# Optimization experiments

Hardware: AMD Instinct MI355X
Metric: run time of the kernel (lower is better)

Reference implementation:

```python
import jax, jax.numpy as jnp
import numpy as np

MAG = 1.0
TAU = 0.5
B, D, C = 8192, 256, 128


def setup_inputs() -> dict:
    key = jax.random.key(0)
    k1, k2 = jax.random.split(key)
    outputs = jax.random.normal(k1, (B, D), dtype=jnp.float32)
    labels = jax.random.normal(k2, (B, C), dtype=jnp.float32)
    return {"outputs": outputs, "labels": labels}


def reference(outputs, labels):
    # Cosine-similarity matrix of labels, min-max normalized to [0, 1]
    norm2labels = labels / (jnp.linalg.norm(labels, axis=1, keepdims=True) + 1e-12)
    sim_mat = norm2labels @ norm2labels.T  # [B, B]
    sim_mat = (sim_mat - sim_mat.min()) / (sim_mat.max() - sim_mat.min())

    # Pairwise Euclidean distances of outputs via the Gram trick
    # ||x_i - x_j||^2 = ||x_i||^2 + ||x_j||^2 - 2 <x_i, x_j>
    sq = jnp.sum(outputs * outputs, axis=1)  # [B]
    d2 = sq[:, None] + sq[None, :] - 2.0 * (outputs @ outputs.T)  # [B, B]
    d2 = jnp.maximum(d2, 0.0)
    nz = d2 > 0.0
    # safe sqrt: zero (diagonal) entries get distance 0 with zero gradient,
    # matching torch.norm's subgradient at 0
    eud = jnp.sqrt(jnp.where(nz, d2, 1.0)) * nz
    eud = eud / eud.max()

    distance = eud + sim_mat  # [B, B]
    pos_mask = sim_mat > TAU

    # Per-row masked log-sum-exp terms (distance in [0, 2], no overflow risk)
    pos_loss = jnp.log(jnp.sum(jnp.where(pos_mask, jnp.exp(distance), 0.0), axis=1))
    neg_loss = jnp.log(jnp.sum(jnp.where(pos_mask, 0.0, jnp.exp(MAG - distance)), axis=1))

    # clamp negatives (and -inf from empty masks) to 0, as the original `if < 0` does
    loss = jnp.maximum(pos_loss, 0.0) + jnp.maximum(neg_loss, 0.0)
    return jnp.mean(loss)
```

## Files before the change

kernel.cpp:

```cpp
#include <hip/hip_runtime.h>
#include <hip/hip_bf16.h>


#define B_N 8192
#define NT   64
#define TILE 128
#define NTRI 2080

typedef __attribute__((ext_vector_type(8))) short bf16x8;
typedef __attribute__((ext_vector_type(4))) float f32x4;
typedef __attribute__((ext_vector_type(2))) _Float16 f16x2;

typedef const __attribute__((address_space(1))) void g_void;
typedef __attribute__((address_space(3))) void l_void;

__device__ __forceinline__ unsigned fenc(float f) {
    unsigned u = __float_as_uint(f);
    return (u & 0x80000000u) ? ~u : (u | 0x80000000u);
}
__device__ __forceinline__ float fdec(unsigned k) {
    unsigned u = (k & 0x80000000u) ? (k ^ 0x80000000u) : ~k;
    return __uint_as_float(u);
}
__device__ __forceinline__ unsigned pack2(float a, float b) {
    f16x2 p; p[0] = (_Float16)a; p[1] = (_Float16)b;
    return *(unsigned*)&p;
}

__device__ __forceinline__ void tile_decode(int b, int& bi, int& bj) {
    int si, sj, ti, tj;
    if (b < 544) {
        int sb = b / 136, w = b - sb * 136;
        int i = 0;
        while (w >= 16 - i) { w -= 16 - i; i++; }
        si = sb; sj = sb; ti = i; tj = i + w;
    } else {
        int q = (b - 544) >> 8, w = (b - 544) & 255;
        int i = 0;
        while (q >= 3 - i) { q -= 3 - i; i++; }
        si = i; sj = i + 1 + q;
        ti = w >> 4; tj = w & 15;
    }
    bi = si * 16 + ti; bj = sj * 16 + tj;
}

__global__ __launch_bounds__(256) void prep_kernel(
    const float* __restrict__ outputs, const float* __restrict__ labels,
    __hip_bfloat16* __restrict__ Obp, __hip_bfloat16* __restrict__ Lnp,
    float* __restrict__ sq, float* __restrict__ pos_sums,
    float* __restrict__ neg_sums, unsigned* __restrict__ stats) {
    int g = blockIdx.x, tid = threadIdx.x;
    int rl = tid >> 4, c = tid & 15;
    int row = g * 16 + rl;
    __shared__ __align__(16) short tO[16][264];
    __shared__ __align__(16) short tL[16][136];

    float s = 0.f;
    #pragma unroll
    for (int k = 0; k < 4; k++) {
        f32x4 v = *(const f32x4*)&outputs[(size_t)row * 256 + c * 16 + k * 4];
        s += v[0]*v[0] + v[1]*v[1] + v[2]*v[2] + v[3]*v[3];
        __hip_bfloat16 b4[4];
        #pragma unroll
        for (int i = 0; i < 4; i++) b4[i] = __float2bfloat16(v[i]);
        *(uint2*)&tO[rl][c * 16 + k * 4] = *(uint2*)b4;
    }
    #pragma unroll
    for (int m = 1; m < 16; m <<= 1) s += __shfl_xor(s, m);
    if (c == 0) sq[row] = s;

    float ls = 0.f;
    f32x4 u0 = *(const f32x4*)&labels[(size_t)row * 128 + c * 8];
    f32x4 u1 = *(const f32x4*)&labels[(size_t)row * 128 + c * 8 + 4];
    ls += u0[0]*u0[0] + u0[1]*u0[1] + u0[2]*u0[2] + u0[3]*u0[3];
    ls += u1[0]*u1[0] + u1[1]*u1[1] + u1[2]*u1[2] + u1[3]*u1[3];
    #pragma unroll
    for (int m = 1; m < 16; m <<= 1) ls += __shfl_xor(ls, m);
    float inv = 1.f / (sqrtf(ls) + 1e-12f);
    {
        __hip_bfloat16 b4[4];
        #pragma unroll
        for (int i = 0; i < 4; i++) b4[i] = __float2bfloat16(u0[i] * inv);
        *(uint2*)&tL[rl][c * 8] = *(uint2*)b4;
        #pragma unroll
        for (int i = 0; i < 4; i++) b4[i] = __float2bfloat16(u1[i] * inv);
        *(uint2*)&tL[rl][c * 8 + 4] = *(uint2*)b4;
    }
    if (tid < 16) { pos_sums[g * 16 + tid] = 0.f; neg_sums[g * 16 + tid] = 0.f; }
    if (g == 0 && tid == 0) {
        stats[0] = 0xFFFFFFFFu; stats[1] = 0u; stats[2] = 0u;
    }
    __syncthreads();

    #pragma unroll
    for (int q = 0; q < 2; q++) {
        int sl = tid * 2 + q;
        int o = sl >> 4, rr = sl & 15;
        uint4 d = *(uint4*)&tO[rr][o * 8];
        *(uint4*)&Obp[(size_t)g * 4096 + (size_t)sl * 8] = d;
    }
    {
        int o = tid >> 4, rr = tid & 15;
        uint4 d = *(uint4*)&tL[rr][o * 8];
        *(uint4*)&Lnp[(size_t)g * 2048 + (size_t)tid * 8] = d;
    }
}

template<int KD8>
__device__ __forceinline__ void stage_slice(
    const short* __restrict__ P, int g0, int o0, short* L, int tid) {
    #pragma unroll
    for (int p = 0; p < 4; p++) {
        int u = p * 256 + tid;
        int gl = u >> 7, off = u & 127;
        size_t gu = ((size_t)(g0 + gl) * KD8 + o0) * 16 + off;
        __builtin_amdgcn_global_load_lds((g_void*)(P + gu * 8),
                                         (l_void*)(L + (size_t)u * 8), 16, 0, 0);
    }
}

__device__ __forceinline__ void mfma_slice(
    const short* As, const short* Bs, int wm4, int wn4,
    int l15, int quad, f32x4 (&acc)[4][4]) {
    #pragma unroll
    for (int kc = 0; kc < 2; kc++) {
        bf16x8 a[4], b[4];
        #pragma unroll
        for (int mi = 0; mi < 4; mi++)
            a[mi] = *(const bf16x8*)&As[((wm4 + mi) * 128
                                         + (kc * 4 + quad) * 16 + l15) * 8];
        #pragma unroll
        for (int ni = 0; ni < 4; ni++)
            b[ni] = *(const bf16x8*)&Bs[((wn4 + ni) * 128
                                         + (kc * 4 + quad) * 16 + l15) * 8];
        #pragma unroll
        for (int mi = 0; mi < 4; mi++)
            #pragma unroll
            for (int ni = 0; ni < 4; ni++)
                acc[mi][ni] = __builtin_amdgcn_mfma_f32_16x16x32_bf16(
                    a[mi], b[ni], acc[mi][ni], 0, 0, 0);
    }
}

__device__ __forceinline__ void zero_acc(f32x4 (&acc)[4][4]) {
    #pragma unroll
    for (int mi = 0; mi < 4; mi++)
        #pragma unroll
        for (int ni = 0; ni < 4; ni++) {
            f32x4 z = {0.f, 0.f, 0.f, 0.f};
            acc[mi][ni] = z;
        }
}

template<int KD8, int NS>
__device__ __forceinline__ void gram_staged(
    const short* __restrict__ P, int gA0, int gB0,
    short* As, short* Bs, int tid, int wm4, int wn4,
    int l15, int quad, f32x4 (&acc)[4][4]) {
    #pragma unroll
    for (int s = 0; s < NS; s++) {
        __syncthreads();
        stage_slice<KD8>(P, gA0, s * 8, As, tid);
        stage_slice<KD8>(P, gB0, s * 8, Bs, tid);
        __syncthreads();
        mfma_slice(As, Bs, wm4, wn4, l15, quad, acc);
    }
}

__global__ __launch_bounds__(256, 2) void stats_kernel(
    const short* __restrict__ Lnp, const short* __restrict__ Obp,
    const float* __restrict__ sq, unsigned* __restrict__ stats) {
    int bi, bj;
    tile_decode(blockIdx.x, bi, bj);
    int tid = threadIdx.x, lane = tid & 63, wid = tid >> 6;
    int wm = (wid >> 1) * 64, wn = (wid & 1) * 64;
    int wm4 = (wid >> 1) * 4, wn4 = (wid & 1) * 4;
    int l15 = lane & 15, quad = lane >> 4;
    int rB = bi * TILE, cB = bj * TILE;

    __shared__ __align__(16) short As[1024 * 8];
    __shared__ __align__(16) short Bs[1024 * 8];

    float lmin = 1e30f, lmax = -1e30f, dmax = 0.f;
    f32x4 acc[4][4];

    zero_acc(acc);
    gram_staged<16, 2>(Lnp, bi * 8, bj * 8, As, Bs, tid, wm4, wn4, l15, quad, acc);
    #pragma unroll
    for (int mi = 0; mi < 4; mi++)
        #pragma unroll
        for (int ni = 0; ni < 4; ni++)
            #pragma unroll
            for (int r = 0; r < 4; r++) {
                float s = acc[mi][ni][r];
                lmin = fminf(lmin, s);
                lmax = fmaxf(lmax, s);
            }

    zero_acc(acc);
    gram_staged<32, 4>(Obp, bi * 8, bj * 8, As, Bs, tid, wm4, wn4, l15, quad, acc);
    float sqj[4];
    #pragma unroll
    for (int ni = 0; ni < 4; ni++) sqj[ni] = sq[cB + wn + ni * 16 + l15];
    #pragma unroll
    for (int mi = 0; mi < 4; mi++) {
        f32x4 sqi = *(const f32x4*)&sq[rB + wm + mi * 16 + quad * 4];
        #pragma unroll
        for (int r = 0; r < 4; r++)
            #pragma unroll
            for (int ni = 0; ni < 4; ni++) {
                float d2 = fmaxf(sqi[r] + sqj[ni] - 2.f * acc[mi][ni][r], 0.f);
                dmax = fmaxf(dmax, d2);
            }
    }

    #pragma unroll
    for (int m = 1; m < 64; m <<= 1) {
        lmin = fminf(lmin, __shfl_xor(lmin, m));
        lmax = fmaxf(lmax, __shfl_xor(lmax, m));
        dmax = fmaxf(dmax, __shfl_xor(dmax, m));
    }
    __shared__ float red[3][4];
    if ((tid & 63) == 0) { red[0][wid] = lmin; red[1][wid] = lmax; red[2][wid] = dmax; }
    __syncthreads();
    if (tid == 0) {
        lmin = fminf(fminf(red[0][0], red[0][1]), fminf(red[0][2], red[0][3]));
        lmax = fmaxf(fmaxf(red[1][0], red[1][1]), fmaxf(red[1][2], red[1][3]));
        dmax = fmaxf(fmaxf(red[2][0], red[2][1]), fmaxf(red[2][2], red[2][3]));
        atomicMin(&stats[0], fenc(lmin));
        atomicMax(&stats[1], fenc(lmax));
        atomicMax(&stats[2], fenc(dmax));
    }
}

__global__ __launch_bounds__(256, 2) void loss_kernel(
    const short* __restrict__ Lnp, const short* __restrict__ Obp,
    const float* __restrict__ sq, const unsigned* __restrict__ stats,
    float* __restrict__ pos_sums, float* __restrict__ neg_sums) {
    int bi, bj;
    tile_decode(blockIdx.x, bi, bj);
    int tid = threadIdx.x, lane = tid & 63, wid = tid >> 6;
    int wm = (wid >> 1) * 64, wn = (wid & 1) * 64;
    int wm4 = (wid >> 1) * 4, wn4 = (wid & 1) * 4;
    int l15 = lane & 15, quad = lane >> 4;
    int rB = bi * TILE, cB = bj * TILE;

    __shared__ __align__(16) short As[1024 * 8];
    __shared__ __align__(16) short Bs[1024 * 8];
    __shared__ unsigned simW[256 * 33];
    __shared__ float rP[TILE][2], rN[TILE][2];
    __shared__ float cP[TILE][2], cN[TILE][2];
    unsigned* my = &simW[tid * 33];

    f32x4 acc[4][4];

    zero_acc(acc);
    gram_staged<16, 2>(Lnp, bi * 8, bj * 8, As, Bs, tid, wm4, wn4, l15, quad, acc);
    #pragma unroll
    for (int mi = 0; mi < 4; mi++)
        #pragma unroll
        for (int ni = 0; ni < 4; ni++) {
            my[(mi * 4 + ni) * 2 + 0] = pack2(acc[mi][ni][0], acc[mi][ni][1]);
            my[(mi * 4 + ni) * 2 + 1] = pack2(acc[mi][ni][2], acc[mi][ni][3]);
        }

    zero_acc(acc);
    gram_staged<32, 4>(Obp, bi * 8, bj * 8, As, Bs, tid, wm4, wn4, l15, quad, acc);

    float smin = fdec(stats[0]);
    float smax = fdec(stats[1]);
    float d2max = fdec(stats[2]);
    float invr = 1.f / (smax - smin);
    float invem = rsqrtf(d2max);

    float sqj[4];
    #pragma unroll
    for (int ni = 0; ni < 4; ni++) sqj[ni] = sq[cB + wn + ni * 16 + l15];
    float cpsum[4] = {0.f, 0.f, 0.f, 0.f};
    float cnsum[4] = {0.f, 0.f, 0.f, 0.f};

    #pragma unroll
    for (int mi = 0; mi < 4; mi++) {
        f32x4 sqi = *(const f32x4*)&sq[rB + wm + mi * 16 + quad * 4];
        float ps[4] = {0.f, 0.f, 0.f, 0.f};
        float ns[4] = {0.f, 0.f, 0.f, 0.f};
        #pragma unroll
        for (int ni = 0; ni < 4; ni++) {
            f16x2 s01 = ((const f16x2*)my)[(mi * 4 + ni) * 2 + 0];
            f16x2 s23 = ((const f16x2*)my)[(mi * 4 + ni) * 2 + 1];
            #pragma unroll
            for (int r = 0; r < 4; r++) {
                float sraw = (r < 2) ? (float)s01[r] : (float)s23[r - 2];
                float sn = (sraw - smin) * invr;
                float g = acc[mi][ni][r];
                float d2 = fmaxf(sqi[r] + sqj[ni] - 2.f * g, 0.f);
                float eud = (d2 > 0.f) ? sqrtf(d2) * invem : 0.f;
                float dist = eud + sn;
                bool pos = sn > 0.5f;
                float pv = pos ? __expf(dist) : 0.f;
                float nv = pos ? 0.f : __expf(1.0f - dist);
                ps[r] += pv;  ns[r] += nv;
                cpsum[ni] += pv;  cnsum[ni] += nv;
            }
        }
        #pragma unroll
        for (int r = 0; r < 4; r++) {
            #pragma unroll
            for (int m = 1; m < 16; m <<= 1) {
                ps[r] += __shfl_xor(ps[r], m);
                ns[r] += __shfl_xor(ns[r], m);
            }
            if (l15 == 0) {
                int rr = wm + mi * 16 + quad * 4 + r;
                rP[rr][wid & 1] = ps[r];
                rN[rr][wid & 1] = ns[r];
            }
        }
    }
    #pragma unroll
    for (int ni = 0; ni < 4; ni++) {
        #pragma unroll
        for (int m = 16; m < 64; m <<= 1) {
            cpsum[ni] += __shfl_xor(cpsum[ni], m);
            cnsum[ni] += __shfl_xor(cnsum[ni], m);
        }
        if (quad == 0) {
            int cc = wn + ni * 16 + l15;
            cP[cc][wid >> 1] = cpsum[ni];
            cN[cc][wid >> 1] = cnsum[ni];
        }
    }
    __syncthreads();
    if (tid < TILE) {
        atomicAdd(&pos_sums[bi * TILE + tid], rP[tid][0] + rP[tid][1]);
        atomicAdd(&neg_sums[bi * TILE + tid], rN[tid][0] + rN[tid][1]);
        if (bi != bj) {
            atomicAdd(&pos_sums[bj * TILE + tid], cP[tid][0] + cP[tid][1]);
            atomicAdd(&neg_sums[bj * TILE + tid], cN[tid][0] + cN[tid][1]);
        }
    }
}

__global__ __launch_bounds__(256) void finalize_kernel(
    const float* __restrict__ pos_sums, const float* __restrict__ neg_sums,
    float* __restrict__ out) {
    int t = threadIdx.x;
    float acc = 0.f;
    for (int i = t; i < B_N; i += 256) {
        float p = pos_sums[i], n = neg_sums[i];
        float pl = fmaxf(logf(p), 0.f);
        float nl = (n > 0.f) ? fmaxf(logf(n), 0.f) : 0.f;
        acc += pl + nl;
    }
    #pragma unroll
    for (int m = 1; m < 64; m <<= 1) acc += __shfl_xor(acc, m);
    __shared__ float w4[4];
    if ((t & 63) == 0) w4[t >> 6] = acc;
    __syncthreads();
    if (t == 0) out[0] = (w4[0] + w4[1] + w4[2] + w4[3]) / (float)B_N;
}

extern "C" void kernel_launch(void* const* d_in, const int* in_sizes, int n_in,
                              void* d_out, int out_size, void* d_ws, size_t ws_size,
                              hipStream_t stream) {
    const float* outputs = (const float*)d_in[0];
    const float* labels  = (const float*)d_in[1];
    float* out = (float*)d_out;
    char* ws = (char*)d_ws;
    __hip_bfloat16* Obp = (__hip_bfloat16*)(ws);
    __hip_bfloat16* Lnp = (__hip_bfloat16*)(ws + 4194304);
    float* sq           = (float*)(ws + 6291456);
    float* pos_sums     = (float*)(ws + 6324224);
    float* neg_sums     = (float*)(ws + 6356992);
    unsigned* stats     = (unsigned*)(ws + 6389760);

    prep_kernel<<<B_N / 16, 256, 0, stream>>>(outputs, labels, Obp, Lnp, sq,
                                              pos_sums, neg_sums, stats);
    stats_kernel<<<NTRI, 256, 0, stream>>>((const short*)Lnp, (const short*)Obp,
                                           sq, stats);
    loss_kernel<<<NTRI, 256, 0, stream>>>((const short*)Lnp, (const short*)Obp,
                                          sq, stats, pos_sums, neg_sums);
    finalize_kernel<<<1, 256, 0, stream>>>(pos_sums, neg_sums, out);
}
```

Before: 241.3 us.

## Cache fp16 sim and distance tiles in stats pass, stream them in loss pass

```diff
diff --git a/kernel.cpp b/kernel.cpp
--- a/kernel.cpp
+++ b/kernel.cpp
@@ -6,10 +6,12 @@
 #define NT   64
 #define TILE 128
 #define NTRI 2080
+#define WS_NEEDED 142704704ull
 
 typedef __attribute__((ext_vector_type(8))) short bf16x8;
 typedef __attribute__((ext_vector_type(4))) float f32x4;
 typedef __attribute__((ext_vector_type(2))) _Float16 f16x2;
+typedef __attribute__((ext_vector_type(4))) unsigned u32x4;
 
 typedef const __attribute__((address_space(1))) void g_void;
 typedef __attribute__((address_space(3))) void l_void;
@@ -169,7 +171,8 @@
 
 __global__ __launch_bounds__(256, 2) void stats_kernel(
     const short* __restrict__ Lnp, const short* __restrict__ Obp,
-    const float* __restrict__ sq, unsigned* __restrict__ stats) {
+    const float* __restrict__ sq, unsigned* __restrict__ stats,
+    unsigned* __restrict__ simT, unsigned* __restrict__ eudT, int store) {
     int bi, bj;
     tile_decode(blockIdx.x, bi, bj);
     int tid = threadIdx.x, lane = tid & 63, wid = tid >> 6;
@@ -177,6 +180,7 @@
     int wm4 = (wid >> 1) * 4, wn4 = (wid & 1) * 4;
     int l15 = lane & 15, quad = lane >> 4;
     int rB = bi * TILE, cB = bj * TILE;
+    size_t tB = (size_t)blockIdx.x * 8192 + (size_t)tid * 4;
 
     __shared__ __align__(16) short As[1024 * 8];
     __shared__ __align__(16) short Bs[1024 * 8];
@@ -187,15 +191,24 @@
     zero_acc(acc);
     gram_staged<16, 2>(Lnp, bi * 8, bj * 8, As, Bs, tid, wm4, wn4, l15, quad, acc);
     #pragma unroll
-    for (int mi = 0; mi < 4; mi++)
+    for (int mi = 0; mi < 4; mi++) {
+        u32x4 v0, v1;
         #pragma unroll
         for (int ni = 0; ni < 4; ni++)
             #pragma unroll
-            for (int r = 0; r < 4; r++) {
-                float s = acc[mi][ni][r];
-                lmin = fminf(lmin, s);
-                lmax = fmaxf(lmax, s);
-            }
+            for (int h = 0; h < 2; h++) {
+                float s0 = acc[mi][ni][2 * h], s1 = acc[mi][ni][2 * h + 1];
+                lmin = fminf(lmin, fminf(s0, s1));
+                lmax = fmaxf(lmax, fmaxf(s0, s1));
+                int j = ni * 2 + h;
+                unsigned pk = pack2(s0, s1);
+                if (j < 4) v0[j] = pk; else v1[j - 4] = pk;
+            }
+        if (store) {
+            __builtin_nontemporal_store(v0, (u32x4*)(simT + tB + (mi * 2 + 0) * 1024));
+            __builtin_nontemporal_store(v1, (u32x4*)(simT + tB + (mi * 2 + 1) * 1024));
+        }
+    }
 
     zero_acc(acc);
     gram_staged<32, 4>(Obp, bi * 8, bj * 8, As, Bs, tid, wm4, wn4, l15, quad, acc);
@@ -205,13 +218,24 @@
     #pragma unroll
     for (int mi = 0; mi < 4; mi++) {
         f32x4 sqi = *(const f32x4*)&sq[rB + wm + mi * 16 + quad * 4];
-        #pragma unroll
-        for (int r = 0; r < 4; r++)
-            #pragma unroll
-            for (int ni = 0; ni < 4; ni++) {
-                float d2 = fmaxf(sqi[r] + sqj[ni] - 2.f * acc[mi][ni][r], 0.f);
-                dmax = fmaxf(dmax, d2);
-            }
+        u32x4 v0, v1;
+        #pragma unroll
+        for (int ni = 0; ni < 4; ni++)
+            #pragma unroll
+            for (int h = 0; h < 2; h++) {
+                float d20 = fmaxf(sqi[2*h]   + sqj[ni] - 2.f * acc[mi][ni][2*h],   0.f);
+                float d21 = fmaxf(sqi[2*h+1] + sqj[ni] - 2.f * acc[mi][ni][2*h+1], 0.f);
+                dmax = fmaxf(dmax, fmaxf(d20, d21));
+                float e0 = (d20 > 0.f) ? sqrtf(d20) : 0.f;
+                float e1 = (d21 > 0.f) ? sqrtf(d21) : 0.f;
+                int j = ni * 2 + h;
+                unsigned pk = pack2(e0, e1);
+                if (j < 4) v0[j] = pk; else v1[j - 4] = pk;
+            }
+        if (store) {
+            __builtin_nontemporal_store(v0, (u32x4*)(eudT + tB + (mi * 2 + 0) * 1024));
+            __builtin_nontemporal_store(v1, (u32x4*)(eudT + tB + (mi * 2 + 1) * 1024));
+        }
     }
 
     #pragma unroll
@@ -233,7 +257,93 @@
     }
 }
 
-__global__ __launch_bounds__(256, 2) void loss_kernel(
+__global__ __launch_bounds__(256) void loss_stream_kernel(
+    const unsigned* __restrict__ simT, const unsigned* __restrict__ eudT,
+    const unsigned* __restrict__ stats,
+    float* __restrict__ pos_sums, float* __restrict__ neg_sums) {
+    int bi, bj;
+    tile_decode(blockIdx.x, bi, bj);
+    int tid = threadIdx.x, lane = tid & 63, wid = tid >> 6;
+    int wm = (wid >> 1) * 64, wn = (wid & 1) * 64;
+    int l15 = lane & 15, quad = lane >> 4;
+    size_t tB = (size_t)blockIdx.x * 8192 + (size_t)tid * 4;
+
+    float smin = fdec(stats[0]);
+    float smax = fdec(stats[1]);
+    float d2max = fdec(stats[2]);
+    float invr = 1.f / (smax - smin);
+    float invem = rsqrtf(d2max);
+
+    __shared__ float rP[TILE][2], rN[TILE][2];
+    __shared__ float cP[TILE][2], cN[TILE][2];
+    float cpsum[4] = {0.f, 0.f, 0.f, 0.f};
+    float cnsum[4] = {0.f, 0.f, 0.f, 0.f};
+
+    #pragma unroll
+    for (int mi = 0; mi < 4; mi++) {
+        u32x4 s0 = __builtin_nontemporal_load((const u32x4*)(simT + tB + (mi * 2 + 0) * 1024));
+        u32x4 s1 = __builtin_nontemporal_load((const u32x4*)(simT + tB + (mi * 2 + 1) * 1024));
+        u32x4 e0 = __builtin_nontemporal_load((const u32x4*)(eudT + tB + (mi * 2 + 0) * 1024));
+        u32x4 e1 = __builtin_nontemporal_load((const u32x4*)(eudT + tB + (mi * 2 + 1) * 1024));
+        float ps[4] = {0.f, 0.f, 0.f, 0.f};
+        float ns[4] = {0.f, 0.f, 0.f, 0.f};
+        #pragma unroll
+        for (int j = 0; j < 8; j++) {
+            unsigned sv = (j < 4) ? s0[j] : s1[j - 4];
+            unsigned ev = (j < 4) ? e0[j] : e1[j - 4];
+            int ni = j >> 1, h = j & 1;
+            f16x2 spair = *(f16x2*)&sv;
+            f16x2 epair = *(f16x2*)&ev;
+            #pragma unroll
+            for (int e = 0; e < 2; e++) {
+                float sn = ((float)spair[e] - smin) * invr;
+                float dist = (float)epair[e] * invem + sn;
+                bool pos = sn > 0.5f;
+                float pv = pos ? __expf(dist) : 0.f;
+                float nv = pos ? 0.f : __expf(1.0f - dist);
+                ps[2 * h + e] += pv;  ns[2 * h + e] += nv;
+                cpsum[ni] += pv;  cnsum[ni] += nv;
+            }
+        }
+        #pragma unroll
+        for (int r = 0; r < 4; r++) {
+            #pragma unroll
+            for (int m = 1; m < 16; m <<= 1) {
+                ps[r] += __shfl_xor(ps[r], m);
+                ns[r] += __shfl_xor(ns[r], m);
+            }
+            if (l15 == 0) {
+                int rr = wm + mi * 16 + quad * 4 + r;
+                rP[rr][wid & 1] = ps[r];
+                rN[rr][wid & 1] = ns[r];
+            }
+        }
+    }
+    #pragma unroll
+    for (int ni = 0; ni < 4; ni++) {
+        #pragma unroll
+        for (int m = 16; m < 64; m <<= 1) {
+            cpsum[ni] += __shfl_xor(cpsum[ni], m);
+            cnsum[ni] += __shfl_xor(cnsum[ni], m);
+        }
+        if (quad == 0) {
+            int cc = wn + ni * 16 + l15;
+            cP[cc][wid >> 1] = cpsum[ni];
+            cN[cc][wid >> 1] = cnsum[ni];
+        }
+    }
+    __syncthreads();
+    if (tid < TILE) {
+        atomicAdd(&pos_sums[bi * TILE + tid], rP[tid][0] + rP[tid][1]);
+        atomicAdd(&neg_sums[bi * TILE + tid], rN[tid][0] + rN[tid][1]);
+        if (bi != bj) {
+            atomicAdd(&pos_sums[bj * TILE + tid], cP[tid][0] + cP[tid][1]);
+            atomicAdd(&neg_sums[bj * TILE + tid], cN[tid][0] + cN[tid][1]);
+        }
+    }
+}
+
+__global__ __launch_bounds__(256, 2) void loss_recompute_kernel(
     const short* __restrict__ Lnp, const short* __restrict__ Obp,
     const float* __restrict__ sq, const unsigned* __restrict__ stats,
     float* __restrict__ pos_sums, float* __restrict__ neg_sums) {
@@ -373,12 +483,21 @@
     float* pos_sums     = (float*)(ws + 6324224);
     float* neg_sums     = (float*)(ws + 6356992);
     unsigned* stats     = (unsigned*)(ws + 6389760);
+    unsigned* simT      = (unsigned*)(ws + 6389824);
+    unsigned* eudT      = (unsigned*)(ws + 74547264);
+    int big = (ws_size >= WS_NEEDED) ? 1 : 0;
 
     prep_kernel<<<B_N / 16, 256, 0, stream>>>(outputs, labels, Obp, Lnp, sq,
                                               pos_sums, neg_sums, stats);
     stats_kernel<<<NTRI, 256, 0, stream>>>((const short*)Lnp, (const short*)Obp,
-                                           sq, stats);
-    loss_kernel<<<NTRI, 256, 0, stream>>>((const short*)Lnp, (const short*)Obp,
-                                          sq, stats, pos_sums, neg_sums);
+                                           sq, stats, simT, eudT, big);
+    if (big)
+        loss_stream_kernel<<<NTRI, 256, 0, stream>>>(simT, eudT, stats,
+                                                     pos_sums, neg_sums);
+    else
+        loss_recompute_kernel<<<NTRI, 256, 0, stream>>>((const short*)Lnp,
+                                                        (const short*)Obp,
+                                                        sq, stats,
+                                                        pos_sums, neg_sums);
     finalize_kernel<<<1, 256, 0, stream>>>(pos_sums, neg_sums, out);
 }
```

New measurement: 206.3 us. -14.5%, faster.
